# Performance work log

Hardware: AMD Instinct MI355X
Metric: run time of the kernel (lower is better)

## Reference

```python
import jax, jax.numpy as jnp
import numpy as np

B, N = 4096, 2048


def setup_inputs() -> dict:
    key = jax.random.key(0)
    k1, k2, k3 = jax.random.split(key, 3)
    target = jax.random.normal(k1, (B, N, 3), dtype=jnp.float32)
    source = jax.random.normal(k2, (B, N, 3), dtype=jnp.float32)
    weights = jax.random.uniform(k3, (B, N, 1), dtype=jnp.float32)
    return {"target": target, "source": source, "weights": weights}


def reference(target, source, weights):
    # Weighted means over the point axis (weights is not None branch of torch code;
    # the isnan mask is unused in that branch).
    wsum = jnp.sum(weights, axis=-2, keepdims=True) + 1e-8  # [B,1,1]
    mean_s = jnp.sum(source * weights, axis=-2, keepdims=True) / wsum  # [B,1,3]
    mean_t = jnp.sum(target * weights, axis=-2, keepdims=True) / wsum  # [B,1,3]
    xyz_tc = (target - mean_t) * weights  # weighted centered target [B,N,3]
    xyz_sc = source - mean_s              # centered source [B,N,3]
    # Cross-covariance: cov = xyz_tc^T @ xyz_sc -> [B,3,3]
    cov = jnp.einsum("bni,bnj->bij", xyz_tc, xyz_sc)
    u, s, vh = jnp.linalg.svd(cov, full_matrices=False)
    rot = u @ vh  # [B,3,3] (no reflection fix, matching original)
    t = jnp.swapaxes(mean_t, -1, -2) - rot @ jnp.swapaxes(mean_s, -1, -2)  # [B,3,1]
    T = jnp.zeros(target.shape[:-2] + (4, 4), dtype=target.dtype)
    T = T.at[..., :3, :3].set(rot)
    T = T.at[..., :3, 3:].set(t)
    T = T.at[..., 3, 3].set(jnp.asarray(1.0, target.dtype))
    return T
```

## Files before the change

kernel.cpp:

```cpp
#include <hip/hip_runtime.h>
#include <math.h>


constexpr int BN = 2048;

template <int SPLIT>
__global__ __launch_bounds__(256) void moments_kernel(
    const float* __restrict__ target,
    const float* __restrict__ source,
    const float* __restrict__ weights,
    float* __restrict__ ws)
{
    const int lane = threadIdx.x & 63;
    const int wid  = blockIdx.x * 4 + (threadIdx.x >> 6);
    const int b    = wid / SPLIT;
    const int part = wid % SPLIT;

    constexpr int GROUPS = BN / 4;
    constexpr int ITERS  = GROUPS / (SPLIT * 64);

    const float4* t4 = reinterpret_cast<const float4*>(target + (size_t)b * BN * 3);
    const float4* s4 = reinterpret_cast<const float4*>(source + (size_t)b * BN * 3);
    const float4* w4 = reinterpret_cast<const float4*>(weights + (size_t)b * BN);
    const int pg0 = part * (GROUPS / SPLIT);

    float acc[16];
#pragma unroll
    for (int i = 0; i < 16; ++i) acc[i] = 0.f;

#pragma unroll
    for (int it = 0; it < ITERS; ++it) {
        const int g = pg0 + it * 64 + lane;
        float4 t0 = t4[g * 3 + 0], t1 = t4[g * 3 + 1], t2 = t4[g * 3 + 2];
        float4 s0 = s4[g * 3 + 0], s1 = s4[g * 3 + 1], s2 = s4[g * 3 + 2];
        float4 wv = w4[g];

        float tx[4] = {t0.x, t0.w, t1.z, t2.y};
        float ty[4] = {t0.y, t1.x, t1.w, t2.z};
        float tz[4] = {t0.z, t1.y, t2.x, t2.w};
        float sx[4] = {s0.x, s0.w, s1.z, s2.y};
        float sy[4] = {s0.y, s1.x, s1.w, s2.z};
        float sz[4] = {s0.z, s1.y, s2.x, s2.w};
        float ww[4] = {wv.x, wv.y, wv.z, wv.w};

#pragma unroll
        for (int j = 0; j < 4; ++j) {
            float w = ww[j];
            acc[0] += w;
            float wtx = w * tx[j], wty = w * ty[j], wtz = w * tz[j];
            acc[1] += wtx;  acc[2] += wty;  acc[3] += wtz;
            acc[4] += w * sx[j]; acc[5] += w * sy[j]; acc[6] += w * sz[j];
            acc[7]  += wtx * sx[j]; acc[8]  += wtx * sy[j]; acc[9]  += wtx * sz[j];
            acc[10] += wty * sx[j]; acc[11] += wty * sy[j]; acc[12] += wty * sz[j];
            acc[13] += wtz * sx[j]; acc[14] += wtz * sy[j]; acc[15] += wtz * sz[j];
        }
    }

    {
        const bool u5 = (lane & 32) != 0;
#pragma unroll
        for (int v = 0; v < 8; ++v) {
            float send = u5 ? acc[v] : acc[v + 8];
            float r = __shfl_xor(send, 32);
            acc[v] = (u5 ? acc[v + 8] : acc[v]) + r;
        }
        const bool u4 = (lane & 16) != 0;
#pragma unroll
        for (int v = 0; v < 4; ++v) {
            float send = u4 ? acc[v] : acc[v + 4];
            float r = __shfl_xor(send, 16);
            acc[v] = (u4 ? acc[v + 4] : acc[v]) + r;
        }
        const bool u3 = (lane & 8) != 0;
#pragma unroll
        for (int v = 0; v < 2; ++v) {
            float send = u3 ? acc[v] : acc[v + 2];
            float r = __shfl_xor(send, 8);
            acc[v] = (u3 ? acc[v + 2] : acc[v]) + r;
        }
        const bool u2 = (lane & 4) != 0;
        {
            float send = u2 ? acc[0] : acc[1];
            float r = __shfl_xor(send, 4);
            acc[0] = (u2 ? acc[1] : acc[0]) + r;
        }
        acc[0] += __shfl_xor(acc[0], 2);
        acc[0] += __shfl_xor(acc[0], 1);
    }

    const int aidx = (((lane >> 5) & 1) << 3) | (((lane >> 4) & 1) << 2) |
                     (((lane >> 3) & 1) << 1) | ((lane >> 2) & 1);
    if ((lane & 3) == 0)
        ws[((size_t)b * SPLIT + part) * 16 + aidx] = acc[0];
}

template <int SPLIT>
__global__ __launch_bounds__(256) void polar_kernel(
    const float* __restrict__ ws,
    float* __restrict__ out,
    int B)
{
    const int b = blockIdx.x * 256 + threadIdx.x;
    if (b >= B) return;

    double v[16];
#pragma unroll
    for (int i = 0; i < 16; ++i) v[i] = 0.0;
#pragma unroll
    for (int p = 0; p < SPLIT; ++p) {
        const float4* i4 = reinterpret_cast<const float4*>(ws + ((size_t)b * SPLIT + p) * 16);
        float4 p0 = i4[0], p1 = i4[1], p2 = i4[2], p3 = i4[3];
        float f[16] = {p0.x, p0.y, p0.z, p0.w,  p1.x, p1.y, p1.z, p1.w,
                       p2.x, p2.y, p2.z, p2.w,  p3.x, p3.y, p3.z, p3.w};
#pragma unroll
        for (int i = 0; i < 16; ++i) v[i] += (double)f[i];
    }

    const double W  = v[0];
    const double Wd = W + 1e-8;
    double St[3] = {v[1], v[2], v[3]};
    double Ss[3] = {v[4], v[5], v[6]};
    double mt[3], ms[3];
#pragma unroll
    for (int i = 0; i < 3; ++i) { mt[i] = St[i] / Wd; ms[i] = Ss[i] / Wd; }

    double A[3][3];
#pragma unroll
    for (int i = 0; i < 3; ++i)
#pragma unroll
        for (int j = 0; j < 3; ++j)
            A[i][j] = v[7 + i * 3 + j] - mt[i] * Ss[j] - ms[j] * St[i] + mt[i] * ms[j] * W;

    double X[3][3];
#pragma unroll
    for (int i = 0; i < 3; ++i)
#pragma unroll
        for (int j = 0; j < 3; ++j) X[i][j] = A[i][j];

#pragma unroll
    for (int iter = 0; iter < 12; ++iter) {
        double C[3][3];
        C[0][0] = X[1][1]*X[2][2] - X[1][2]*X[2][1];
        C[0][1] = X[1][2]*X[2][0] - X[1][0]*X[2][2];
        C[0][2] = X[1][0]*X[2][1] - X[1][1]*X[2][0];
        C[1][0] = X[0][2]*X[2][1] - X[0][1]*X[2][2];
        C[1][1] = X[0][0]*X[2][2] - X[0][2]*X[2][0];
        C[1][2] = X[0][1]*X[2][0] - X[0][0]*X[2][1];
        C[2][0] = X[0][1]*X[1][2] - X[0][2]*X[1][1];
        C[2][1] = X[0][2]*X[1][0] - X[0][0]*X[1][2];
        C[2][2] = X[0][0]*X[1][1] - X[0][1]*X[1][0];
        double det = X[0][0]*C[0][0] + X[0][1]*C[0][1] + X[0][2]*C[0][2];
        double ad  = fabs(det);
        if (!(ad > 1e-300)) { det = (det >= 0.0) ? 1e-300 : -1e-300; ad = 1e-300; }

        double mu = 1.0;
        if (iter < 9) {
            float adf = (float)ad;
            if (adf > 0.f && isfinite(adf))
                mu = (double)exp2f(-log2f(adf) * (1.0f / 3.0f));
        }
        double k1 = 0.5 * mu;
        double k2 = 0.5 / (mu * det);
#pragma unroll
        for (int i = 0; i < 3; ++i)
#pragma unroll
            for (int j = 0; j < 3; ++j)
                X[i][j] = k1 * X[i][j] + k2 * C[i][j];
    }

    double tvec[3];
#pragma unroll
    for (int i = 0; i < 3; ++i) {
        double s = mt[i];
#pragma unroll
        for (int k = 0; k < 3; ++k) s -= X[i][k] * ms[k];
        tvec[i] = s;
    }

    float4* o = reinterpret_cast<float4*>(out + (size_t)b * 16);
    o[0] = make_float4((float)X[0][0], (float)X[0][1], (float)X[0][2], (float)tvec[0]);
    o[1] = make_float4((float)X[1][0], (float)X[1][1], (float)X[1][2], (float)tvec[1]);
    o[2] = make_float4((float)X[2][0], (float)X[2][1], (float)X[2][2], (float)tvec[2]);
    o[3] = make_float4(0.f, 0.f, 0.f, 1.f);
}

extern "C" void kernel_launch(void* const* d_in, const int* in_sizes, int n_in,
                              void* d_out, int out_size, void* d_ws, size_t ws_size,
                              hipStream_t stream) {
    const float* target  = (const float*)d_in[0];
    const float* source  = (const float*)d_in[1];
    const float* weights = (const float*)d_in[2];
    float* out = (float*)d_out;
    float* ws  = (float*)d_ws;

    const int B = in_sizes[2] / BN;

    if (ws_size >= (size_t)B * 2 * 16 * sizeof(float)) {
        moments_kernel<2><<<B * 2 / 4, 256, 0, stream>>>(target, source, weights, ws);
        polar_kernel<2><<<(B + 255) / 256, 256, 0, stream>>>(ws, out, B);
    } else {
        moments_kernel<1><<<B / 4, 256, 0, stream>>>(target, source, weights, ws);
        polar_kernel<1><<<(B + 255) / 256, 256, 0, stream>>>(ws, out, B);
    }
}
```

Baseline: 43.62 us.

## Fuse moments and polar kernels into one block-per-batch kernel with prefetch

Replaces the two-kernel pipeline (moments into a workspace, then a per-batch polar decomposition) with one kernel. Each 128-thread block handles one batch: its two wavefronts reduce through shared memory, then thread 0 runs the polar iteration. Loads are software-pipelined by prefetching the next iteration's float4s into registers, and the Newton polar iterations drop from 12 to 10 with fewer scaled steps. This removes a launch and the workspace round trip. The cost is a serial double-precision tail on one thread per block, which may leave the CU idle, and a possible accuracy loss from fewer iterations.

New measurement: 43.88 us, median of 2. Within noise of the previous version (+0.6%).

```diff
diff --git a/kernel.cpp b/kernel.cpp
--- a/kernel.cpp
+++ b/kernel.cpp
@@ -4,44 +4,50 @@
 
 constexpr int BN = 2048;
 
-template <int SPLIT>
-__global__ __launch_bounds__(256) void moments_kernel(
+__global__ __launch_bounds__(128) void svdreg_fused(
     const float* __restrict__ target,
     const float* __restrict__ source,
     const float* __restrict__ weights,
-    float* __restrict__ ws)
+    float* __restrict__ out)
 {
     const int lane = threadIdx.x & 63;
-    const int wid  = blockIdx.x * 4 + (threadIdx.x >> 6);
-    const int b    = wid / SPLIT;
-    const int part = wid % SPLIT;
+    const int wav  = threadIdx.x >> 6;
+    const int b    = blockIdx.x;
 
     constexpr int GROUPS = BN / 4;
-    constexpr int ITERS  = GROUPS / (SPLIT * 64);
+    constexpr int GPW    = GROUPS / 2;
+    constexpr int ITERS  = GPW / 64;
 
     const float4* t4 = reinterpret_cast<const float4*>(target + (size_t)b * BN * 3);
     const float4* s4 = reinterpret_cast<const float4*>(source + (size_t)b * BN * 3);
     const float4* w4 = reinterpret_cast<const float4*>(weights + (size_t)b * BN);
-    const int pg0 = part * (GROUPS / SPLIT);
 
     float acc[16];
 #pragma unroll
     for (int i = 0; i < 16; ++i) acc[i] = 0.f;
 
+    int g = wav * GPW + lane;
+    float4 ct0 = t4[g * 3 + 0], ct1 = t4[g * 3 + 1], ct2 = t4[g * 3 + 2];
+    float4 cs0 = s4[g * 3 + 0], cs1 = s4[g * 3 + 1], cs2 = s4[g * 3 + 2];
+    float4 cwv = w4[g];
+
 #pragma unroll
     for (int it = 0; it < ITERS; ++it) {
-        const int g = pg0 + it * 64 + lane;
-        float4 t0 = t4[g * 3 + 0], t1 = t4[g * 3 + 1], t2 = t4[g * 3 + 2];
-        float4 s0 = s4[g * 3 + 0], s1 = s4[g * 3 + 1], s2 = s4[g * 3 + 2];
-        float4 wv = w4[g];
+        float4 nt0, nt1, nt2, ns0, ns1, ns2, nwv;
+        if (it + 1 < ITERS) {
+            const int gn = g + 64;
+            nt0 = t4[gn * 3 + 0]; nt1 = t4[gn * 3 + 1]; nt2 = t4[gn * 3 + 2];
+            ns0 = s4[gn * 3 + 0]; ns1 = s4[gn * 3 + 1]; ns2 = s4[gn * 3 + 2];
+            nwv = w4[gn];
+        }
 
-        float tx[4] = {t0.x, t0.w, t1.z, t2.y};
-        float ty[4] = {t0.y, t1.x, t1.w, t2.z};
-        float tz[4] = {t0.z, t1.y, t2.x, t2.w};
-        float sx[4] = {s0.x, s0.w, s1.z, s2.y};
-        float sy[4] = {s0.y, s1.x, s1.w, s2.z};
-        float sz[4] = {s0.z, s1.y, s2.x, s2.w};
-        float ww[4] = {wv.x, wv.y, wv.z, wv.w};
+        float tx[4] = {ct0.x, ct0.w, ct1.z, ct2.y};
+        float ty[4] = {ct0.y, ct1.x, ct1.w, ct2.z};
+        float tz[4] = {ct0.z, ct1.y, ct2.x, ct2.w};
+        float sx[4] = {cs0.x, cs0.w, cs1.z, cs2.y};
+        float sy[4] = {cs0.y, cs1.x, cs1.w, cs2.z};
+        float sz[4] = {cs0.z, cs1.y, cs2.x, cs2.w};
+        float ww[4] = {cwv.x, cwv.y, cwv.z, cwv.w};
 
 #pragma unroll
         for (int j = 0; j < 4; ++j) {
@@ -54,6 +60,10 @@
             acc[10] += wty * sx[j]; acc[11] += wty * sy[j]; acc[12] += wty * sz[j];
             acc[13] += wtz * sx[j]; acc[14] += wtz * sy[j]; acc[15] += wtz * sz[j];
         }
+
+        ct0 = nt0; ct1 = nt1; ct2 = nt2;
+        cs0 = ns0; cs1 = ns1; cs2 = ns2;
+        cwv = nwv; g += 64;
     }
 
     {
@@ -88,33 +98,18 @@
         acc[0] += __shfl_xor(acc[0], 1);
     }
 
+    __shared__ float part[2][16];
     const int aidx = (((lane >> 5) & 1) << 3) | (((lane >> 4) & 1) << 2) |
                      (((lane >> 3) & 1) << 1) | ((lane >> 2) & 1);
-    if ((lane & 3) == 0)
-        ws[((size_t)b * SPLIT + part) * 16 + aidx] = acc[0];
-}
+    if ((lane & 3) == 0) part[wav][aidx] = acc[0];
+    __syncthreads();
 
-template <int SPLIT>
-__global__ __launch_bounds__(256) void polar_kernel(
-    const float* __restrict__ ws,
-    float* __restrict__ out,
-    int B)
-{
-    const int b = blockIdx.x * 256 + threadIdx.x;
-    if (b >= B) return;
+    if (threadIdx.x != 0) return;
 
     double v[16];
 #pragma unroll
-    for (int i = 0; i < 16; ++i) v[i] = 0.0;
-#pragma unroll
-    for (int p = 0; p < SPLIT; ++p) {
-        const float4* i4 = reinterpret_cast<const float4*>(ws + ((size_t)b * SPLIT + p) * 16);
-        float4 p0 = i4[0], p1 = i4[1], p2 = i4[2], p3 = i4[3];
-        float f[16] = {p0.x, p0.y, p0.z, p0.w,  p1.x, p1.y, p1.z, p1.w,
-                       p2.x, p2.y, p2.z, p2.w,  p3.x, p3.y, p3.z, p3.w};
-#pragma unroll
-        for (int i = 0; i < 16; ++i) v[i] += (double)f[i];
-    }
+    for (int i = 0; i < 16; ++i)
+        v[i] = (double)part[0][i] + (double)part[1][i];
 
     const double W  = v[0];
     const double Wd = W + 1e-8;
@@ -138,7 +133,7 @@
         for (int j = 0; j < 3; ++j) X[i][j] = A[i][j];
 
 #pragma unroll
-    for (int iter = 0; iter < 12; ++iter) {
+    for (int iter = 0; iter < 10; ++iter) {
         double C[3][3];
         C[0][0] = X[1][1]*X[2][2] - X[1][2]*X[2][1];
         C[0][1] = X[1][2]*X[2][0] - X[1][0]*X[2][2];
@@ -154,7 +149,7 @@
         if (!(ad > 1e-300)) { det = (det >= 0.0) ? 1e-300 : -1e-300; ad = 1e-300; }
 
         double mu = 1.0;
-        if (iter < 9) {
+        if (iter < 6) {
             float adf = (float)ad;
             if (adf > 0.f && isfinite(adf))
                 mu = (double)exp2f(-log2f(adf) * (1.0f / 3.0f));
@@ -191,15 +186,7 @@
     const float* source  = (const float*)d_in[1];
     const float* weights = (const float*)d_in[2];
     float* out = (float*)d_out;
-    float* ws  = (float*)d_ws;
 
     const int B = in_sizes[2] / BN;
-
-    if (ws_size >= (size_t)B * 2 * 16 * sizeof(float)) {
-        moments_kernel<2><<<B * 2 / 4, 256, 0, stream>>>(target, source, weights, ws);
-        polar_kernel<2><<<(B + 255) / 256, 256, 0, stream>>>(ws, out, B);
-    } else {
-        moments_kernel<1><<<B / 4, 256, 0, stream>>>(target, source, weights, ws);
-        polar_kernel<1><<<(B + 255) / 256, 256, 0, stream>>>(ws, out, B);
-    }
+    svdreg_fused<<<B, 128, 0, stream>>>(target, source, weights, out);
 }
```
